# Kernel optimization log

Measured on AMD Instinct MI355X. Metric: run time of the kernel, lower is better.

Reference implementation:

```python
import jax, jax.numpy as jnp
import numpy as np
import math

B, S, D, H, M, R = 4, 1024, 1024, 16, 4, 64
DH = D // H
EPS = 1e-8

def setup_inputs() -> dict:
    key = jax.random.key(0)
    ks = jax.random.split(key, 8)
    sc = 0.02
    return {
        'x': jax.random.normal(ks[0], (B, S, D), jnp.float32),
        'Wk': jax.random.normal(ks[1], (D, D), jnp.float32) * sc,
        'bk': jnp.zeros((D,), jnp.float32),
        'Wq': jax.random.normal(ks[2], (D, D), jnp.float32) * sc,
        'bq': jnp.zeros((D,), jnp.float32),
        'Wv': jax.random.normal(ks[3], (D, D), jnp.float32) * sc,
        'bv': jnp.zeros((D,), jnp.float32),
        'mask1': jax.random.normal(ks[4], (M, R, S), jnp.float32) * sc,
        'mask2': jax.random.normal(ks[5], (M, R, S), jnp.float32) * sc,
        'roll_back': jax.random.randint(ks[6], (M, S, S), 0, S, jnp.int64),
    }

def reference(x, Wk, bk, Wq, bq, Wv, bv, mask1, mask2, roll_back):
    def proj(W, b):
        # torch Linear: x @ W^T + b ; reshape to [B, H, S, DH]
        y = jnp.dot(x, W.T) + b
        return y.reshape(B, S, H, DH).transpose(0, 2, 1, 3)
    k = proj(Wk, bk)
    q = proj(Wq, bq)
    v = proj(Wv, bv)
    # learnable low-rank mask: [M, S, S]
    learnable_mask = jnp.einsum('mrs,mrt->mst', mask1, mask2)
    # gather along last dim with roll_back indices
    gathered = jnp.take_along_axis(learnable_mask, roll_back, axis=-1)  # [M, S, S]
    att = jnp.einsum('bhsd,bhtd->bhst', q, k) / math.sqrt(DH)  # [B, H, S, S]
    att = att.reshape(B, H // M, M, S, S) * gathered[None, None]
    att = att.reshape(B, H, S, S)
    # Frobenius norm over last two dims per (B, H)
    fro = jnp.sqrt(jnp.sum(att * att, axis=(-2, -1), keepdims=True))
    att = att / (fro + EPS)
    out = jnp.einsum('bhst,bhtd->bhsd', att, v)
    return out.transpose(0, 2, 1, 3).reshape(B, S, D)
```

## Files before the change

### kernel.cpp

```cpp
#include <hip/hip_runtime.h>
#include <hip/hip_bf16.h>
#include <stdint.h>

typedef __attribute__((ext_vector_type(8))) __bf16 bf16x8;
typedef __attribute__((ext_vector_type(4))) float  f32x4;

__device__ __forceinline__ ushort f2bf(float f) {
    union { float f; uint32_t u; } v; v.f = f;
    uint32_t u = v.u;
    uint32_t r = 0x7FFFu + ((u >> 16) & 1u);
    return (ushort)((u + r) >> 16);
}
__device__ __forceinline__ float bf2f(ushort u) {
    union { uint32_t u; float f; } v; v.u = ((uint32_t)u) << 16;
    return v.f;
}
__device__ __forceinline__ uint32_t pack2bf(float a, float b) {
    return (uint32_t)f2bf(a) | ((uint32_t)f2bf(b) << 16);
}

typedef __attribute__((address_space(3))) uint32_t lds_u32_t;
typedef const __attribute__((address_space(1))) uint32_t glb_u32_t;
__device__ __forceinline__ void async_copy16(const void* g, void* l) {
    __builtin_amdgcn_global_load_lds((glb_u32_t*)g, (lds_u32_t*)l, 16, 0, 0);
}

__global__ __launch_bounds__(256) void prep(
    const float* __restrict__ x, const float* __restrict__ wk,
    const float* __restrict__ wq, const float* __restrict__ wv,
    const float* __restrict__ m1, const float* __restrict__ m2,
    const int* __restrict__ rb,
    ushort* __restrict__ xb, ushort* __restrict__ wball, ushort* __restrict__ gth)
{
    __shared__ float As8[64 * 8];
    __shared__ float lmS[8 * 1024];
    const int tid = threadIdx.x;
    if (blockIdx.x >= 512) {
        int i = (blockIdx.x - 512) * 256 + tid;
        const float* src; ushort* dst; int j;
        if (i < 1048576) { src = x; dst = xb; j = i; }
        else {
            int t = i - 1048576;
            int z = t >> 18;
            j = t & 262143;
            src = (z == 0) ? wk : (z == 1) ? wq : wv;
            dst = wball + z * 1048576;
        }
        float4 f = ((const float4*)src)[j];
        ushort4 o;
        o.x = f2bf(f.x); o.y = f2bf(f.y); o.z = f2bf(f.z); o.w = f2bf(f.w);
        ((ushort4*)dst)[j] = o;
        return;
    }
    const int s0 = (blockIdx.x & 127) * 8;
    const int m = blockIdx.x >> 7;
    if (tid < 128) {
        int r = tid >> 1, half = tid & 1;
        *(float4*)&As8[r * 8 + half * 4] =
            *(const float4*)&m1[(m * 64 + r) * 1024 + s0 + half * 4];
    }
    __syncthreads();
    f32x4 acc8[8];
    #pragma unroll
    for (int s = 0; s < 8; s++) acc8[s] = (f32x4){0.f, 0.f, 0.f, 0.f};
    const float* m2b = m2 + m * 65536 + tid * 4;
    #pragma unroll 4
    for (int r = 0; r < 64; r++) {
        float4 b4 = *(const float4*)&m2b[r * 1024];
        f32x4 b = (f32x4){b4.x, b4.y, b4.z, b4.w};
        #pragma unroll
        for (int s = 0; s < 8; s++) acc8[s] += As8[r * 8 + s] * b;
    }
    #pragma unroll
    for (int s = 0; s < 8; s++)
        *(f32x4*)&lmS[s * 1024 + tid * 4] = acc8[s];
    __syncthreads();
    const int base = (m * 1024 + s0) * 1024;
    #pragma unroll
    for (int i = 0; i < 8; i++) {
        int c = tid + i * 256;
        int row = c >> 8, j = (c & 255) * 4;
        int4 idx = *(const int4*)&rb[base + row * 1024 + j];
        ushort4 o;
        o.x = f2bf(lmS[row * 1024 + (idx.x & 1023)] * 0.125f);
        o.y = f2bf(lmS[row * 1024 + (idx.y & 1023)] * 0.125f);
        o.z = f2bf(lmS[row * 1024 + (idx.z & 1023)] * 0.125f);
        o.w = f2bf(lmS[row * 1024 + (idx.w & 1023)] * 0.125f);
        *(ushort4*)&gth[base + row * 1024 + j] = o;
    }
}

__global__ __launch_bounds__(256, 2) void proj_gemm(
    const ushort* __restrict__ xb, const ushort* __restrict__ wball,
    const float* __restrict__ bk, const float* __restrict__ bq, const float* __restrict__ bv,
    ushort* __restrict__ kd, ushort* __restrict__ qd, ushort* __restrict__ vd)
{
    __shared__ ushort As[2][128 * 64];
    __shared__ ushort Bs[2][128 * 64];
    const int g = blockIdx.x;
    const int col0 = (g & 7) * 128;
    const int t = g >> 3;
    const int row0 = (t & 31) * 128;
    const int z = t >> 5;
    const ushort* wb = wball + z * 1048576;
    const int tid = threadIdx.x;
    const int lane = tid & 63, wave = tid >> 6;
    const int quad = lane >> 4, m15 = lane & 15;
    const int wr = wave >> 1, wc = wave & 1;

    f32x4 acc[4][4];
    for (int i = 0; i < 4; i++)
        for (int j = 0; j < 4; j++) acc[i][j] = (f32x4){0.f, 0.f, 0.f, 0.f};

    auto stage = [&](int buf, int kk) {
        #pragma unroll
        for (int i = 0; i < 4; i++) {
            int c = tid + i * 256;
            int r = c >> 3, cjp = c & 7;
            int cj = cjp ^ (r & 7);
            async_copy16(&xb[(row0 + r) * 1024 + kk + cj * 8], &As[buf][c * 8]);
            async_copy16(&wb[(col0 + r) * 1024 + kk + cj * 8], &Bs[buf][c * 8]);
        }
    };

    stage(0, 0);
    for (int it = 0; it < 16; it++) {
        __syncthreads();
        if (it < 15) stage((it + 1) & 1, (it + 1) * 64);
        const ushort* Ab = As[it & 1];
        const ushort* Bb = Bs[it & 1];
        #pragma unroll
        for (int kh = 0; kh < 2; kh++) {
            bf16x8 af[4], bfv[4];
            #pragma unroll
            for (int fr = 0; fr < 4; fr++) {
                int row = wr * 64 + fr * 16 + m15;
                int q4 = kh * 4 + quad;
                af[fr] = *(const bf16x8*)&Ab[row * 64 + ((q4 ^ (row & 7)) * 8)];
            }
            #pragma unroll
            for (int fc = 0; fc < 4; fc++) {
                int row = wc * 64 + fc * 16 + m15;
                int q4 = kh * 4 + quad;
                bfv[fc] = *(const bf16x8*)&Bs[it & 1][row * 64 + ((q4 ^ (row & 7)) * 8)];
            }
            #pragma unroll
            for (int fr = 0; fr < 4; fr++)
                #pragma unroll
                for (int fc = 0; fc < 4; fc++)
                    acc[fr][fc] = __builtin_amdgcn_mfma_f32_16x16x32_bf16(af[fr], bfv[fc], acc[fr][fc], 0, 0, 0);
        }
    }

    const float* bias = (z == 0) ? bk : (z == 1) ? bq : bv;
    ushort* dstA = (z == 0) ? kd : qd;
    for (int fr = 0; fr < 4; fr++) {
        int ibase = row0 + wr * 64 + fr * 16 + quad * 4;
        int b_ = ibase >> 10, s = ibase & 1023;
        for (int fc = 0; fc < 4; fc++) {
            int j = col0 + wc * 64 + fc * 16 + m15;
            int h = j >> 6, dh = j & 63;
            float bb = bias[j];
            if (z < 2) {
                for (int r = 0; r < 4; r++)
                    dstA[((b_ * 16 + h) * 1024 + (s + r)) * 64 + dh] = f2bf(acc[fr][fc][r] + bb);
            } else {
                ushort4 o;
                o.x = f2bf(acc[fr][fc][0] + bb);
                o.y = f2bf(acc[fr][fc][1] + bb);
                o.z = f2bf(acc[fr][fc][2] + bb);
                o.w = f2bf(acc[fr][fc][3] + bb);
                *(ushort4*)&vd[((b_ * 16 + h) * 64 + dh) * 1024 + s] = o;
            }
        }
    }
}

__global__ __launch_bounds__(256, 2) void attention(
    const ushort* __restrict__ qd, const ushort* __restrict__ kd, const ushort* __restrict__ vd,
    const ushort* __restrict__ gth, float* __restrict__ O, float* __restrict__ ss)
{
    __shared__ ushort Ks[2][64 * 64];
    __shared__ ushort Vs[2][64 * 64];
    __shared__ ushort Ms[2][64 * 64];
    __shared__ ushort Ps[64 * 72];
    __shared__ float Osc[64 * 68];
    __shared__ float red[4];
    const int g = blockIdx.x;
    const int idx = g >> 3;
    const int s0 = (idx & 15) * 64;
    const int bh = (g & 7) + 8 * (idx >> 4);
    const int mm = bh & 3;
    const int tid = threadIdx.x, lane = tid & 63, wave = tid >> 6;
    const int quad = lane >> 4, m15 = lane & 15;
    const int sw = wave * 16 + m15;
    const int sw7 = m15 & 7;
    const ushort* gbase = gth + mm * 1048576 + s0 * 1024;

    #pragma unroll
    for (int i = 0; i < 2; i++) {
        int c = tid + i * 256;
        int r = c >> 3, cj = (c & 7) ^ (r & 7);
        async_copy16(&qd[(bh * 1024 + s0 + r) * 64 + cj * 8], &Ks[0][c * 8]);
    }
    __syncthreads();
    bf16x8 qf[2];
    #pragma unroll
    for (int kk = 0; kk < 2; kk++)
        qf[kk] = *(const bf16x8*)&Ks[0][sw * 64 + (((kk * 4 + quad) ^ sw7) * 8)];
    __syncthreads();

    f32x4 oacc[4];
    #pragma unroll
    for (int i = 0; i < 4; i++) oacc[i] = (f32x4){0.f, 0.f, 0.f, 0.f};
    float ssacc = 0.f;

    auto stage = [&](int buf, int t0) {
        #pragma unroll
        for (int i = 0; i < 2; i++) {
            int c = tid + i * 256;
            int r = c >> 3, cj = (c & 7) ^ (r & 7);
            async_copy16(&kd[(bh * 1024 + t0 + r) * 64 + cj * 8], &Ks[buf][c * 8]);
            async_copy16(&vd[(bh * 64 + r) * 1024 + t0 + cj * 8], &Vs[buf][c * 8]);
            async_copy16(&gbase[r * 1024 + t0 + cj * 8],          &Ms[buf][c * 8]);
        }
    };

    stage(0, 0);
    for (int it = 0; it < 16; it++) {
        __syncthreads();
        if (it < 15) stage((it + 1) & 1, (it + 1) * 64);
        const ushort* Kb = Ks[it & 1];
        const ushort* Vb = Vs[it & 1];
        const ushort* Mb = Ms[it & 1];

        f32x4 pacc[4];
        #pragma unroll
        for (int tc = 0; tc < 4; tc++) {
            f32x4 p = (f32x4){0.f, 0.f, 0.f, 0.f};
            #pragma unroll
            for (int kk = 0; kk < 2; kk++) {
                int row = tc * 16 + m15;
                bf16x8 a = *(const bf16x8*)&Kb[row * 64 + (((kk * 4 + quad) ^ (row & 7)) * 8)];
                p = __builtin_amdgcn_mfma_f32_16x16x32_bf16(a, qf[kk], p, 0, 0, 0);
            }
            pacc[tc] = p;
        }
        #pragma unroll
        for (int tc = 0; tc < 4; tc++) {
            int ch = (tc * 2 + (quad >> 1)) ^ sw7;
            ushort4 mv4 = *(const ushort4*)&Mb[sw * 64 + ch * 8 + (quad & 1) * 4];
            float p0 = pacc[tc][0] * bf2f(mv4.x);
            float p1 = pacc[tc][1] * bf2f(mv4.y);
            float p2 = pacc[tc][2] * bf2f(mv4.z);
            float p3 = pacc[tc][3] * bf2f(mv4.w);
            ssacc += p0 * p0 + p1 * p1 + p2 * p2 + p3 * p3;
            uint2 pw;
            pw.x = pack2bf(p0, p1);
            pw.y = pack2bf(p2, p3);
            *(uint2*)&Ps[sw * 72 + tc * 16 + quad * 4] = pw;
        }
        bf16x8 pf[2];
        #pragma unroll
        for (int kk = 0; kk < 2; kk++)
            pf[kk] = *(const bf16x8*)&Ps[sw * 72 + kk * 32 + quad * 8];
        #pragma unroll
        for (int nc = 0; nc < 4; nc++) {
            #pragma unroll
            for (int kk = 0; kk < 2; kk++) {
                int row = nc * 16 + m15;
                bf16x8 a = *(const bf16x8*)&Vb[row * 64 + (((kk * 4 + quad) ^ (row & 7)) * 8)];
                oacc[nc] = __builtin_amdgcn_mfma_f32_16x16x32_bf16(a, pf[kk], oacc[nc], 0, 0, 0);
            }
        }
    }
    __syncthreads();
    #pragma unroll
    for (int nc = 0; nc < 4; nc++)
        *(f32x4*)&Osc[sw * 68 + nc * 16 + quad * 4] = oacc[nc];
    __syncthreads();
    #pragma unroll
    for (int i = 0; i < 4; i++) {
        int c = tid + i * 256;
        int row = c >> 4, col = (c & 15) * 4;
        f32x4 v4 = *(const f32x4*)&Osc[row * 68 + col];
        *(f32x4*)&O[(bh * 1024 + s0 + row) * 64 + col] = v4;
    }
    for (int off = 32; off; off >>= 1) ssacc += __shfl_down(ssacc, off, 64);
    if (lane == 0) red[wave] = ssacc;
    __syncthreads();
    if (tid == 0) atomicAdd(&ss[bh], red[0] + red[1] + red[2] + red[3]);
}

__global__ __launch_bounds__(256) void normalize_out(const float* __restrict__ O,
                                                     const float* __restrict__ ss,
                                                     float* __restrict__ out)
{
    int gid = blockIdx.x * 256 + threadIdx.x;
    int e = gid * 4;
    int bh = e >> 16;
    float inv = 1.f / (sqrtf(ss[bh]) + 1e-8f);
    float4 v4 = *(const float4*)&O[e];
    int b_ = bh >> 4, h = bh & 15;
    int s = (e >> 6) & 1023, dh = e & 63;
    float4 o4 = {v4.x * inv, v4.y * inv, v4.z * inv, v4.w * inv};
    *(float4*)&out[((b_ * 1024 + s) * 16 + h) * 64 + dh] = o4;
}

extern "C" void kernel_launch(void* const* d_in, const int* in_sizes, int n_in,
                              void* d_out, int out_size, void* d_ws, size_t ws_size,
                              hipStream_t stream) {
    const float* x  = (const float*)d_in[0];
    const float* Wk = (const float*)d_in[1];
    const float* bk = (const float*)d_in[2];
    const float* Wq = (const float*)d_in[3];
    const float* bq = (const float*)d_in[4];
    const float* Wv = (const float*)d_in[5];
    const float* bv = (const float*)d_in[6];
    const float* m1 = (const float*)d_in[7];
    const float* m2 = (const float*)d_in[8];
    const int*   rb = (const int*)d_in[9];
    float* out = (float*)d_out;

    char* ws = (char*)d_ws;
    ushort* xb    = (ushort*)(ws);
    ushort* wball = (ushort*)(ws + 8388608);
    ushort* kd    = (ushort*)(ws + 14680064);
    ushort* qd    = (ushort*)(ws + 23068672);
    ushort* vd    = (ushort*)(ws + 31457280);
    float*  O     = (float*)(ws + 39845888);
    ushort* gth   = (ushort*)(ws + 56623104);
    float*  ssb   = (float*)(ws + 65011712);

    prep<<<7680, 256, 0, stream>>>(x, Wk, Wq, Wv, m1, m2, rb, xb, wball, gth);
    proj_gemm<<<768, 256, 0, stream>>>(xb, wball, bk, bq, bv, kd, qd, vd);
    hipMemsetAsync(ssb, 0, 64 * sizeof(float), stream);
    attention<<<1024, 256, 0, stream>>>(qd, kd, vd, gth, O, ssb);
    normalize_out<<<4096, 256, 0, stream>>>(O, ssb, out);
}
```

Measured before the change: 206.8 us.

## Trim attention epilogue, pack bf16 with perm, fold ss reset into prep

The attention kernel now writes O directly from MFMA accumulators instead of staging through a shared-memory tile. This removes the Osc buffer and two barriers, which lowers LDS use and may raise occupancy. Mask values are loaded before the QK MFMAs, and products use packed f32x2 math. Bf16 packing uses a perm-based round-half-up instead of round-to-nearest-even. The sum-of-squares reset moves from a separate memset into the prep kernel, saving one launch. The direct O store is less coalesced, and the rounding mode changes slightly.

Measured after the change: 207.0 us. No clear change (+0.1%).

```diff
diff --git a/kernel.cpp b/kernel.cpp
--- a/kernel.cpp
+++ b/kernel.cpp
@@ -4,6 +4,7 @@
 
 typedef __attribute__((ext_vector_type(8))) __bf16 bf16x8;
 typedef __attribute__((ext_vector_type(4))) float  f32x4;
+typedef __attribute__((ext_vector_type(2))) float  f32x2;
 
 __device__ __forceinline__ ushort f2bf(float f) {
     union { float f; uint32_t u; } v; v.f = f;
@@ -11,12 +12,13 @@
     uint32_t r = 0x7FFFu + ((u >> 16) & 1u);
     return (ushort)((u + r) >> 16);
 }
-__device__ __forceinline__ float bf2f(ushort u) {
-    union { uint32_t u; float f; } v; v.u = ((uint32_t)u) << 16;
+__device__ __forceinline__ uint32_t pack2(f32x2 v) {
+    union { float f; uint32_t u; } a, b; a.f = v[0]; b.f = v[1];
+    return __builtin_amdgcn_perm(b.u + 0x8000u, a.u + 0x8000u, 0x07060302u);
+}
+__device__ __forceinline__ float u2f(uint32_t u) {
+    union { uint32_t u; float f; } v; v.u = u;
     return v.f;
-}
-__device__ __forceinline__ uint32_t pack2bf(float a, float b) {
-    return (uint32_t)f2bf(a) | ((uint32_t)f2bf(b) << 16);
 }
 
 typedef __attribute__((address_space(3))) uint32_t lds_u32_t;
@@ -30,11 +32,13 @@
     const float* __restrict__ wq, const float* __restrict__ wv,
     const float* __restrict__ m1, const float* __restrict__ m2,
     const int* __restrict__ rb,
-    ushort* __restrict__ xb, ushort* __restrict__ wball, ushort* __restrict__ gth)
+    ushort* __restrict__ xb, ushort* __restrict__ wball, ushort* __restrict__ gth,
+    float* __restrict__ ssb)
 {
     __shared__ float As8[64 * 8];
     __shared__ float lmS[8 * 1024];
     const int tid = threadIdx.x;
+    if (blockIdx.x == 0 && tid < 64) ssb[tid] = 0.f;
     if (blockIdx.x >= 512) {
         int i = (blockIdx.x - 512) * 256 + tid;
         const float* src; ushort* dst; int j;
@@ -142,7 +146,7 @@
             for (int fc = 0; fc < 4; fc++) {
                 int row = wc * 64 + fc * 16 + m15;
                 int q4 = kh * 4 + quad;
-                bfv[fc] = *(const bf16x8*)&Bs[it & 1][row * 64 + ((q4 ^ (row & 7)) * 8)];
+                bfv[fc] = *(const bf16x8*)&Bb[row * 64 + ((q4 ^ (row & 7)) * 8)];
             }
             #pragma unroll
             for (int fr = 0; fr < 4; fr++)
@@ -184,7 +188,6 @@
     __shared__ ushort Vs[2][64 * 64];
     __shared__ ushort Ms[2][64 * 64];
     __shared__ ushort Ps[64 * 72];
-    __shared__ float Osc[64 * 68];
     __shared__ float red[4];
     const int g = blockIdx.x;
     const int idx = g >> 3;
@@ -213,7 +216,7 @@
     f32x4 oacc[4];
     #pragma unroll
     for (int i = 0; i < 4; i++) oacc[i] = (f32x4){0.f, 0.f, 0.f, 0.f};
-    float ssacc = 0.f;
+    f32x2 ss2 = (f32x2){0.f, 0.f};
 
     auto stage = [&](int buf, int t0) {
         #pragma unroll
@@ -234,6 +237,13 @@
         const ushort* Vb = Vs[it & 1];
         const ushort* Mb = Ms[it & 1];
 
+        uint2 mraw[4];
+        #pragma unroll
+        for (int tc = 0; tc < 4; tc++) {
+            int ch = (tc * 2 + (quad >> 1)) ^ sw7;
+            mraw[tc] = *(const uint2*)&Mb[sw * 64 + ch * 8 + (quad & 1) * 4];
+        }
+
         f32x4 pacc[4];
         #pragma unroll
         for (int tc = 0; tc < 4; tc++) {
@@ -248,16 +258,16 @@
         }
         #pragma unroll
         for (int tc = 0; tc < 4; tc++) {
-            int ch = (tc * 2 + (quad >> 1)) ^ sw7;
-            ushort4 mv4 = *(const ushort4*)&Mb[sw * 64 + ch * 8 + (quad & 1) * 4];
-            float p0 = pacc[tc][0] * bf2f(mv4.x);
-            float p1 = pacc[tc][1] * bf2f(mv4.y);
-            float p2 = pacc[tc][2] * bf2f(mv4.z);
-            float p3 = pacc[tc][3] * bf2f(mv4.w);
-            ssacc += p0 * p0 + p1 * p1 + p2 * p2 + p3 * p3;
+            uint2 w = mraw[tc];
+            f32x2 m01 = (f32x2){u2f(w.x << 16), u2f(w.x & 0xFFFF0000u)};
+            f32x2 m23 = (f32x2){u2f(w.y << 16), u2f(w.y & 0xFFFF0000u)};
+            f32x2 p01 = (f32x2){pacc[tc][0], pacc[tc][1]} * m01;
+            f32x2 p23 = (f32x2){pacc[tc][2], pacc[tc][3]} * m23;
+            ss2 += p01 * p01;
+            ss2 += p23 * p23;
             uint2 pw;
-            pw.x = pack2bf(p0, p1);
-            pw.y = pack2bf(p2, p3);
+            pw.x = pack2(p01);
+            pw.y = pack2(p23);
             *(uint2*)&Ps[sw * 72 + tc * 16 + quad * 4] = pw;
         }
         bf16x8 pf[2];
@@ -274,18 +284,11 @@
             }
         }
     }
-    __syncthreads();
     #pragma unroll
     for (int nc = 0; nc < 4; nc++)
-        *(f32x4*)&Osc[sw * 68 + nc * 16 + quad * 4] = oacc[nc];
-    __syncthreads();
-    #pragma unroll
-    for (int i = 0; i < 4; i++) {
-        int c = tid + i * 256;
-        int row = c >> 4, col = (c & 15) * 4;
-        f32x4 v4 = *(const f32x4*)&Osc[row * 68 + col];
-        *(f32x4*)&O[(bh * 1024 + s0 + row) * 64 + col] = v4;
-    }
+        *(f32x4*)&O[(bh * 1024 + s0 + sw) * 64 + nc * 16 + quad * 4] = oacc[nc];
+
+    float ssacc = ss2[0] + ss2[1];
     for (int off = 32; off; off >>= 1) ssacc += __shfl_down(ssacc, off, 64);
     if (lane == 0) red[wave] = ssacc;
     __syncthreads();
@@ -332,9 +335,8 @@
     ushort* gth   = (ushort*)(ws + 56623104);
     float*  ssb   = (float*)(ws + 65011712);
 
-    prep<<<7680, 256, 0, stream>>>(x, Wk, Wq, Wv, m1, m2, rb, xb, wball, gth);
+    prep<<<7680, 256, 0, stream>>>(x, Wk, Wq, Wv, m1, m2, rb, xb, wball, gth, ssb);
     proj_gemm<<<768, 256, 0, stream>>>(xb, wball, bk, bq, bv, kd, qd, vd);
-    hipMemsetAsync(ssb, 0, 64 * sizeof(float), stream);
     attention<<<1024, 256, 0, stream>>>(qd, kd, vd, gth, O, ssb);
     normalize_out<<<4096, 256, 0, stream>>>(O, ssb, out);
 }
```
